# Kernel optimization log

Hardware: AMD Instinct MI355X
Metric: run time of the kernel (lower is better)

## Reference

```python
import jax, jax.numpy as jnp
import numpy as np

B_, N, C = 4096, 49, 128
H = 4          # num_heads
NW = 64        # windows per image


def setup_inputs() -> dict:
    key = jax.random.key(0)
    k = jax.random.split(key, 6)
    s = 0.02
    return {
        "x": jax.random.normal(k[0], (B_, N, C), jnp.float32),
        "mask": jax.random.normal(k[1], (NW, N, N), jnp.float32),
        "qkv_w": jax.random.normal(k[2], (3 * C, C), jnp.float32) * s,
        "qkv_b": jax.random.normal(k[3], (3 * C,), jnp.float32) * s,
        "proj_w": jax.random.normal(k[4], (C, C), jnp.float32) * s,
        "proj_b": jax.random.normal(k[5], (C,), jnp.float32) * s,
    }


def reference(x, mask, qkv_w, qkv_b, proj_w, proj_b):
    b, n, c = x.shape
    hd = c // H
    scale = hd ** -0.5
    # fused QKV projection: [b, n, 3, H, hd] -> [3, b, H, n, hd]
    qkv = (x @ qkv_w.T + qkv_b).reshape(b, n, 3, H, hd)
    qkv = jnp.transpose(qkv, (2, 0, 3, 1, 4))
    q, k, v = qkv[0] * scale, qkv[1], qkv[2]
    attn = jnp.einsum("bhnd,bhmd->bhnm", q, k)  # [b, H, n, n]
    nW = mask.shape[0]
    attn = attn.reshape(b // nW, nW, H, n, n) + mask[None, :, None, :, :]
    attn = jax.nn.softmax(attn.reshape(b, H, n, n), axis=-1)
    out = jnp.einsum("bhnm,bhmd->bhnd", attn, v)
    out = jnp.transpose(out, (0, 2, 1, 3)).reshape(b, n, c)
    return out @ proj_w.T + proj_b
```

## Files before the change

kernel.cpp:

```cpp
#include <hip/hip_runtime.h>
#include <hip/hip_bf16.h>

#define C_DIM 128
#define SCALE 0.17677669529663687f

typedef __attribute__((ext_vector_type(8))) short frag8;
typedef __attribute__((ext_vector_type(4))) float f32x4;
typedef __attribute__((ext_vector_type(4))) unsigned int u32x4;

#define XACT_STR 136
#define VT_BASE 8000
#define VT_PER_HEAD 2304
#define Q_STR 40
#define VT_STR 72
#define SMEM_TOT 17216

__device__ __forceinline__ unsigned short f2b(float x) {
    __hip_bfloat16 h = __float2bfloat16(x);
    return __builtin_bit_cast(unsigned short, h);
}
__device__ __forceinline__ unsigned pk2(float a, float b) {
    return ((unsigned)f2b(b) << 16) | (unsigned)f2b(a);
}
__device__ __forceinline__ void add4(f32x4& a, float4 m) {
    a[0] += m.x; a[1] += m.y; a[2] += m.z; a[3] += m.w;
}

__global__ void convert_weights(const float4* __restrict__ qkvw,
                                const float4* __restrict__ projw,
                                ushort4* __restrict__ wbf) {
    int i = blockIdx.x * 256 + threadIdx.x;
    float4 v = (i < 12288) ? qkvw[i] : projw[i - 12288];
    ushort4 p;
    p.x = f2b(v.x); p.y = f2b(v.y); p.z = f2b(v.z); p.w = f2b(v.w);
    wbf[i] = p;
}

__global__ void pad_mask(const float* __restrict__ mask, float* __restrict__ pm) {
    int t = blockIdx.x * 256 + threadIdx.x;
    int w = t / 784, rem = t % 784, i = rem >> 4, tq = rem & 15;
    const float* src = mask + (size_t)w * 2401 + i * 49;
    int j = tq * 4;
    float4 v;
    v.x = (j     < 49) ? src[j]     : 0.f;
    v.y = (j + 1 < 49) ? src[j + 1] : 0.f;
    v.z = (j + 2 < 49) ? src[j + 2] : 0.f;
    v.w = (j + 3 < 49) ? src[j + 3] : 0.f;
    ((float4*)pm)[t] = v;
}

__global__ __launch_bounds__(256) void attn_mfma(
    const float* __restrict__ x,
    const float* __restrict__ pmask,
    const float* __restrict__ qkv_b,
    const float* __restrict__ proj_b,
    const unsigned short* __restrict__ wq,
    float* __restrict__ out)
{
    __shared__ __align__(16) unsigned short sm[SMEM_TOT];

    const int b = blockIdx.x, tid = threadIdx.x;
    const int h    = tid >> 6;
    const int lane = tid & 63;
    const int n16  = lane & 15;
    const int q    = lane >> 4;

    {
        const float4* xg = (const float4*)(x + (size_t)b * 6272);
        for (int i = tid; i < 1568; i += 256) {
            float4 v = xg[i];
            int row = i >> 5, col = (i & 31) << 2;
            uint2 pk; pk.x = pk2(v.x, v.y); pk.y = pk2(v.z, v.w);
            *(uint2*)&sm[row * XACT_STR + col] = pk;
        }
    }
    __syncthreads();

    frag8 xf[4][4];
#pragma unroll
    for (int tt = 0; tt < 4; ++tt)
#pragma unroll
        for (int ks = 0; ks < 4; ++ks)
            xf[tt][ks] = *(const frag8*)&sm[min(tt * 16 + n16, 48) * XACT_STR + ks * 32 + q * 8];
    __syncthreads();

    const int KB = h * 2000;
    const int VB = VT_BASE + h * VT_PER_HEAD;

#pragma unroll
    for (int ct = 0; ct < 2; ++ct) {
        const unsigned short* wrow = wq + (size_t)(C_DIM + h * 32 + ct * 16 + n16) * C_DIM;
        frag8 wf[4];
#pragma unroll
        for (int ks = 0; ks < 4; ++ks) wf[ks] = *(const frag8*)(wrow + ks * 32 + q * 8);
        float4 b4 = *(const float4*)(qkv_b + C_DIM + h * 32 + ct * 16 + q * 4);
#pragma unroll
        for (int tt = 0; tt < 4; ++tt) {
            f32x4 acc = {0.f, 0.f, 0.f, 0.f};
#pragma unroll
            for (int ks = 0; ks < 4; ++ks)
                acc = __builtin_amdgcn_mfma_f32_16x16x32_bf16(wf[ks], xf[tt][ks], acc, 0, 0, 0);
            uint2 pk;
            pk.x = pk2(acc[0] + b4.x, acc[1] + b4.y);
            pk.y = pk2(acc[2] + b4.z, acc[3] + b4.w);
            *(uint2*)&sm[KB + min(tt * 16 + n16, 49) * Q_STR + ct * 16 + q * 4] = pk;
        }
    }
#pragma unroll
    for (int ct = 0; ct < 2; ++ct) {
        const unsigned short* wrow = wq + (size_t)(2 * C_DIM + h * 32 + ct * 16 + n16) * C_DIM;
        frag8 wf[4];
#pragma unroll
        for (int ks = 0; ks < 4; ++ks) wf[ks] = *(const frag8*)(wrow + ks * 32 + q * 8);
        float bias = qkv_b[2 * C_DIM + h * 32 + ct * 16 + n16];
#pragma unroll
        for (int tt = 0; tt < 4; ++tt) {
            f32x4 acc = {0.f, 0.f, 0.f, 0.f};
#pragma unroll
            for (int ks = 0; ks < 4; ++ks)
                acc = __builtin_amdgcn_mfma_f32_16x16x32_bf16(xf[tt][ks], wf[ks], acc, 0, 0, 0);
            uint2 pk;
            pk.x = pk2(acc[0] + bias, acc[1] + bias);
            pk.y = pk2(acc[2] + bias, acc[3] + bias);
            *(uint2*)&sm[VB + (ct * 16 + n16) * VT_STR + tt * 16 + q * 4] = pk;
        }
    }
    unsigned qw[4][2][2];
#pragma unroll
    for (int ct = 0; ct < 2; ++ct) {
        const unsigned short* wrow = wq + (size_t)(h * 32 + ct * 16 + n16) * C_DIM;
        frag8 wf[4];
#pragma unroll
        for (int ks = 0; ks < 4; ++ks) wf[ks] = *(const frag8*)(wrow + ks * 32 + q * 8);
        float4 b4 = *(const float4*)(qkv_b + h * 32 + ct * 16 + q * 4);
#pragma unroll
        for (int tt = 0; tt < 4; ++tt) {
            f32x4 acc = {0.f, 0.f, 0.f, 0.f};
#pragma unroll
            for (int ks = 0; ks < 4; ++ks)
                acc = __builtin_amdgcn_mfma_f32_16x16x32_bf16(wf[ks], xf[tt][ks], acc, 0, 0, 0);
            qw[tt][ct][0] = pk2((acc[0] + b4.x) * SCALE, (acc[1] + b4.y) * SCALE);
            qw[tt][ct][1] = pk2((acc[2] + b4.z) * SCALE, (acc[3] + b4.w) * SCALE);
        }
    }

    const int srcA = ((q & 1) << 5) + n16;
    const int srcB = srcA + 16;
    const int hi = q >> 1;
    frag8 qf[4];
#pragma unroll
    for (int it = 0; it < 4; ++it) {
        unsigned a00 = __shfl((int)qw[it][0][0], srcA);
        unsigned a10 = __shfl((int)qw[it][1][0], srcA);
        unsigned a01 = __shfl((int)qw[it][0][1], srcA);
        unsigned a11 = __shfl((int)qw[it][1][1], srcA);
        unsigned b00 = __shfl((int)qw[it][0][0], srcB);
        unsigned b10 = __shfl((int)qw[it][1][0], srcB);
        unsigned b01 = __shfl((int)qw[it][0][1], srcB);
        unsigned b11 = __shfl((int)qw[it][1][1], srcB);
        u32x4 t;
        t[0] = hi ? a10 : a00;
        t[1] = hi ? a11 : a01;
        t[2] = hi ? b10 : b00;
        t[3] = hi ? b11 : b01;
        qf[it] = __builtin_bit_cast(frag8, t);
    }

    frag8 kf[4];
#pragma unroll
    for (int t = 0; t < 4; ++t)
        kf[t] = *(const frag8*)&sm[KB + (t * 16 + n16) * Q_STR + q * 8];
    frag8 vf[2][2];
#pragma unroll
    for (int ct = 0; ct < 2; ++ct)
#pragma unroll
        for (int ks = 0; ks < 2; ++ks)
            vf[ct][ks] = *(const frag8*)&sm[VB + (ct * 16 + n16) * VT_STR + ks * 32 + q * 8];
    __syncthreads();

    const float4* pm4 = (const float4*)(pmask + (size_t)(b & 63) * 3136);
    f32x4 o[2][4];
#pragma unroll
    for (int ct = 0; ct < 2; ++ct)
#pragma unroll
        for (int nt = 0; nt < 4; ++nt) o[ct][nt] = (f32x4){0.f, 0.f, 0.f, 0.f};

#pragma unroll
    for (int it = 0; it < 4; ++it) {
        int ii = min(it * 16 + n16, 48);
        float4 mj[4];
#pragma unroll
        for (int jt = 0; jt < 4; ++jt) mj[jt] = pm4[ii * 16 + q + jt * 4];

        f32x4 s4[4];
#pragma unroll
        for (int jt = 0; jt < 4; ++jt) {
            s4[jt] = (f32x4){0.f, 0.f, 0.f, 0.f};
            s4[jt] = __builtin_amdgcn_mfma_f32_16x16x32_bf16(kf[jt], qf[it], s4[jt], 0, 0, 0);
        }
#pragma unroll
        for (int jt = 0; jt < 4; ++jt) add4(s4[jt], mj[jt]);

        float mx = -1e30f;
#pragma unroll
        for (int jt = 0; jt < 4; ++jt)
#pragma unroll
            for (int r = 0; r < 4; ++r)
                if (jt * 16 + q * 4 + r < 49) mx = fmaxf(mx, s4[jt][r]);
        mx = fmaxf(mx, __shfl_xor(mx, 16));
        mx = fmaxf(mx, __shfl_xor(mx, 32));

        float sum = 0.f;
#pragma unroll
        for (int jt = 0; jt < 4; ++jt)
#pragma unroll
            for (int r = 0; r < 4; ++r) {
                float e = (jt * 16 + q * 4 + r < 49) ? __expf(s4[jt][r] - mx) : 0.f;
                s4[jt][r] = e;
                sum += e;
            }
        sum += __shfl_xor(sum, 16);
        sum += __shfl_xor(sum, 32);
        float inv = __builtin_amdgcn_rcpf(sum);

        unsigned pw[4][2];
#pragma unroll
        for (int jt = 0; jt < 4; ++jt) {
            pw[jt][0] = pk2(s4[jt][0], s4[jt][1]);
            pw[jt][1] = pk2(s4[jt][2], s4[jt][3]);
        }
#pragma unroll
        for (int ks = 0; ks < 2; ++ks) {
            unsigned a0  = __shfl((int)pw[2 * ks][0],     srcA);
            unsigned a0h = __shfl((int)pw[2 * ks + 1][0], srcA);
            unsigned a1  = __shfl((int)pw[2 * ks][1],     srcA);
            unsigned a1h = __shfl((int)pw[2 * ks + 1][1], srcA);
            unsigned b0  = __shfl((int)pw[2 * ks][0],     srcB);
            unsigned b0h = __shfl((int)pw[2 * ks + 1][0], srcB);
            unsigned b1  = __shfl((int)pw[2 * ks][1],     srcB);
            unsigned b1h = __shfl((int)pw[2 * ks + 1][1], srcB);
            u32x4 t;
            t[0] = hi ? a0h : a0;
            t[1] = hi ? a1h : a1;
            t[2] = hi ? b0h : b0;
            t[3] = hi ? b1h : b1;
            frag8 pf = __builtin_bit_cast(frag8, t);
#pragma unroll
            for (int ct = 0; ct < 2; ++ct)
                o[ct][it] = __builtin_amdgcn_mfma_f32_16x16x32_bf16(vf[ct][ks], pf, o[ct][it], 0, 0, 0);
        }
#pragma unroll
        for (int ct = 0; ct < 2; ++ct)
#pragma unroll
            for (int r = 0; r < 4; ++r) o[ct][it][r] *= inv;
    }

#pragma unroll
    for (int ct = 0; ct < 2; ++ct)
#pragma unroll
        for (int nt = 0; nt < 4; ++nt) {
            uint2 pk;
            pk.x = pk2(o[ct][nt][0], o[ct][nt][1]);
            pk.y = pk2(o[ct][nt][2], o[ct][nt][3]);
            *(uint2*)&sm[min(nt * 16 + n16, 49) * XACT_STR + h * 32 + ct * 16 + q * 4] = pk;
        }

    const unsigned short* pwq = wq + 49152;
    frag8 wf2[2][4];
#pragma unroll
    for (int ct = 0; ct < 2; ++ct)
#pragma unroll
        for (int ks = 0; ks < 4; ++ks)
            wf2[ct][ks] = *(const frag8*)(pwq + (size_t)(h * 32 + ct * 16 + n16) * C_DIM + ks * 32 + q * 8);
    float4 pb4[2];
#pragma unroll
    for (int ct = 0; ct < 2; ++ct)
        pb4[ct] = *(const float4*)(proj_b + h * 32 + ct * 16 + q * 4);
    __syncthreads();

    float* outb = out + (size_t)b * 6272;
    frag8 af[4][4];
#pragma unroll
    for (int nt = 0; nt < 4; ++nt)
#pragma unroll
        for (int ks = 0; ks < 4; ++ks)
            af[nt][ks] = *(const frag8*)&sm[min(nt * 16 + n16, 48) * XACT_STR + ks * 32 + q * 8];
#pragma unroll
    for (int nt = 0; nt < 4; ++nt) {
        int tok = nt * 16 + n16;
#pragma unroll
        for (int ct = 0; ct < 2; ++ct) {
            f32x4 acc = {0.f, 0.f, 0.f, 0.f};
#pragma unroll
            for (int ks = 0; ks < 4; ++ks)
                acc = __builtin_amdgcn_mfma_f32_16x16x32_bf16(wf2[ct][ks], af[nt][ks], acc, 0, 0, 0);
            if (tok < 49)
                *(float4*)&outb[tok * C_DIM + h * 32 + ct * 16 + q * 4] =
                    make_float4(acc[0] + pb4[ct].x, acc[1] + pb4[ct].y,
                                acc[2] + pb4[ct].z, acc[3] + pb4[ct].w);
        }
    }
}

extern "C" void kernel_launch(void* const* d_in, const int* in_sizes, int n_in,
                              void* d_out, int out_size, void* d_ws, size_t ws_size,
                              hipStream_t stream) {
    const float* x      = (const float*)d_in[0];
    const float* mask   = (const float*)d_in[1];
    const float* qkv_b  = (const float*)d_in[3];
    const float* proj_b = (const float*)d_in[5];

    unsigned short* wbf = (unsigned short*)d_ws;
    float* pmask = (float*)((char*)d_ws + 131072);
    convert_weights<<<64, 256, 0, stream>>>((const float4*)d_in[2],
                                            (const float4*)d_in[4],
                                            (ushort4*)wbf);
    pad_mask<<<196, 256, 0, stream>>>(mask, pmask);
    attn_mfma<<<4096, 256, 0, stream>>>(x, pmask, qkv_b, proj_b, wbf, (float*)d_out);
}
```

Before: 270.0 us.

## Split each head across two wavefronts by token tiles, doubling block size

Each block now runs 512 threads, with two wavefronts per head that each own half of the 16-row token tiles for the QKV projection, attention and output projection. A separate shared-memory region holds the attention output, so it no longer overwrites the x staging area, and a barrier is added after the K/V writes. The aim is more parallelism and latency hiding per window with fewer registers per wave. In exchange, each wave reloads the same weight fragments, more shared memory is used per block, and K/V now have to be exchanged between the two waves.

```diff
diff --git a/kernel.cpp b/kernel.cpp
--- a/kernel.cpp
+++ b/kernel.cpp
@@ -11,9 +11,10 @@
 #define XACT_STR 136
 #define VT_BASE 8000
 #define VT_PER_HEAD 2304
+#define ACT_BASE 17216
 #define Q_STR 40
 #define VT_STR 72
-#define SMEM_TOT 17216
+#define SMEM_TOT 24016
 
 __device__ __forceinline__ unsigned short f2b(float x) {
     __hip_bfloat16 h = __float2bfloat16(x);
@@ -49,7 +50,7 @@
     ((float4*)pm)[t] = v;
 }
 
-__global__ __launch_bounds__(256) void attn_mfma(
+__global__ __launch_bounds__(512) void attn_mfma(
     const float* __restrict__ x,
     const float* __restrict__ pmask,
     const float* __restrict__ qkv_b,
@@ -60,14 +61,17 @@
     __shared__ __align__(16) unsigned short sm[SMEM_TOT];
 
     const int b = blockIdx.x, tid = threadIdx.x;
-    const int h    = tid >> 6;
+    const int w    = tid >> 6;
+    const int h    = w >> 1;
+    const int half = w & 1;
+    const int t0   = half * 2;
     const int lane = tid & 63;
     const int n16  = lane & 15;
     const int q    = lane >> 4;
 
     {
         const float4* xg = (const float4*)(x + (size_t)b * 6272);
-        for (int i = tid; i < 1568; i += 256) {
+        for (int i = tid; i < 1568; i += 512) {
             float4 v = xg[i];
             int row = i >> 5, col = (i & 31) << 2;
             uint2 pk; pk.x = pk2(v.x, v.y); pk.y = pk2(v.z, v.w);
@@ -76,12 +80,12 @@
     }
     __syncthreads();
 
-    frag8 xf[4][4];
-#pragma unroll
-    for (int tt = 0; tt < 4; ++tt)
+    frag8 xf[2][4];
+#pragma unroll
+    for (int il = 0; il < 2; ++il)
 #pragma unroll
         for (int ks = 0; ks < 4; ++ks)
-            xf[tt][ks] = *(const frag8*)&sm[min(tt * 16 + n16, 48) * XACT_STR + ks * 32 + q * 8];
+            xf[il][ks] = *(const frag8*)&sm[min((t0 + il) * 16 + n16, 48) * XACT_STR + ks * 32 + q * 8];
     __syncthreads();
 
     const int KB = h * 2000;
@@ -95,15 +99,15 @@
         for (int ks = 0; ks < 4; ++ks) wf[ks] = *(const frag8*)(wrow + ks * 32 + q * 8);
         float4 b4 = *(const float4*)(qkv_b + C_DIM + h * 32 + ct * 16 + q * 4);
 #pragma unroll
-        for (int tt = 0; tt < 4; ++tt) {
+        for (int il = 0; il < 2; ++il) {
             f32x4 acc = {0.f, 0.f, 0.f, 0.f};
 #pragma unroll
             for (int ks = 0; ks < 4; ++ks)
-                acc = __builtin_amdgcn_mfma_f32_16x16x32_bf16(wf[ks], xf[tt][ks], acc, 0, 0, 0);
+                acc = __builtin_amdgcn_mfma_f32_16x16x32_bf16(wf[ks], xf[il][ks], acc, 0, 0, 0);
             uint2 pk;
             pk.x = pk2(acc[0] + b4.x, acc[1] + b4.y);
             pk.y = pk2(acc[2] + b4.z, acc[3] + b4.w);
-            *(uint2*)&sm[KB + min(tt * 16 + n16, 49) * Q_STR + ct * 16 + q * 4] = pk;
+            *(uint2*)&sm[KB + min((t0 + il) * 16 + n16, 49) * Q_STR + ct * 16 + q * 4] = pk;
         }
     }
 #pragma unroll
@@ -114,18 +118,18 @@
         for (int ks = 0; ks < 4; ++ks) wf[ks] = *(const frag8*)(wrow + ks * 32 + q * 8);
         float bias = qkv_b[2 * C_DIM + h * 32 + ct * 16 + n16];
 #pragma unroll
-        for (int tt = 0; tt < 4; ++tt) {
+        for (int il = 0; il < 2; ++il) {
             f32x4 acc = {0.f, 0.f, 0.f, 0.f};
 #pragma unroll
             for (int ks = 0; ks < 4; ++ks)
-                acc = __builtin_amdgcn_mfma_f32_16x16x32_bf16(xf[tt][ks], wf[ks], acc, 0, 0, 0);
+                acc = __builtin_amdgcn_mfma_f32_16x16x32_bf16(xf[il][ks], wf[ks], acc, 0, 0, 0);
             uint2 pk;
             pk.x = pk2(acc[0] + bias, acc[1] + bias);
             pk.y = pk2(acc[2] + bias, acc[3] + bias);
-            *(uint2*)&sm[VB + (ct * 16 + n16) * VT_STR + tt * 16 + q * 4] = pk;
-        }
-    }
-    unsigned qw[4][2][2];
+            *(uint2*)&sm[VB + (ct * 16 + n16) * VT_STR + (t0 + il) * 16 + q * 4] = pk;
+        }
+    }
+    unsigned qw[2][2][2];
 #pragma unroll
     for (int ct = 0; ct < 2; ++ct) {
         const unsigned short* wrow = wq + (size_t)(h * 32 + ct * 16 + n16) * C_DIM;
@@ -134,36 +138,37 @@
         for (int ks = 0; ks < 4; ++ks) wf[ks] = *(const frag8*)(wrow + ks * 32 + q * 8);
         float4 b4 = *(const float4*)(qkv_b + h * 32 + ct * 16 + q * 4);
 #pragma unroll
-        for (int tt = 0; tt < 4; ++tt) {
+        for (int il = 0; il < 2; ++il) {
             f32x4 acc = {0.f, 0.f, 0.f, 0.f};
 #pragma unroll
             for (int ks = 0; ks < 4; ++ks)
-                acc = __builtin_amdgcn_mfma_f32_16x16x32_bf16(wf[ks], xf[tt][ks], acc, 0, 0, 0);
-            qw[tt][ct][0] = pk2((acc[0] + b4.x) * SCALE, (acc[1] + b4.y) * SCALE);
-            qw[tt][ct][1] = pk2((acc[2] + b4.z) * SCALE, (acc[3] + b4.w) * SCALE);
-        }
-    }
+                acc = __builtin_amdgcn_mfma_f32_16x16x32_bf16(wf[ks], xf[il][ks], acc, 0, 0, 0);
+            qw[il][ct][0] = pk2((acc[0] + b4.x) * SCALE, (acc[1] + b4.y) * SCALE);
+            qw[il][ct][1] = pk2((acc[2] + b4.z) * SCALE, (acc[3] + b4.w) * SCALE);
+        }
+    }
+    __syncthreads();
 
     const int srcA = ((q & 1) << 5) + n16;
     const int srcB = srcA + 16;
     const int hi = q >> 1;
-    frag8 qf[4];
-#pragma unroll
-    for (int it = 0; it < 4; ++it) {
-        unsigned a00 = __shfl((int)qw[it][0][0], srcA);
-        unsigned a10 = __shfl((int)qw[it][1][0], srcA);
-        unsigned a01 = __shfl((int)qw[it][0][1], srcA);
-        unsigned a11 = __shfl((int)qw[it][1][1], srcA);
-        unsigned b00 = __shfl((int)qw[it][0][0], srcB);
-        unsigned b10 = __shfl((int)qw[it][1][0], srcB);
-        unsigned b01 = __shfl((int)qw[it][0][1], srcB);
-        unsigned b11 = __shfl((int)qw[it][1][1], srcB);
+    frag8 qf[2];
+#pragma unroll
+    for (int il = 0; il < 2; ++il) {
+        unsigned a00 = __shfl((int)qw[il][0][0], srcA);
+        unsigned a10 = __shfl((int)qw[il][1][0], srcA);
+        unsigned a01 = __shfl((int)qw[il][0][1], srcA);
+        unsigned a11 = __shfl((int)qw[il][1][1], srcA);
+        unsigned b00 = __shfl((int)qw[il][0][0], srcB);
+        unsigned b10 = __shfl((int)qw[il][1][0], srcB);
+        unsigned b01 = __shfl((int)qw[il][0][1], srcB);
+        unsigned b11 = __shfl((int)qw[il][1][1], srcB);
         u32x4 t;
         t[0] = hi ? a10 : a00;
         t[1] = hi ? a11 : a01;
         t[2] = hi ? b10 : b00;
         t[3] = hi ? b11 : b01;
-        qf[it] = __builtin_bit_cast(frag8, t);
+        qf[il] = __builtin_bit_cast(frag8, t);
     }
 
     frag8 kf[4];
@@ -176,17 +181,17 @@
 #pragma unroll
         for (int ks = 0; ks < 2; ++ks)
             vf[ct][ks] = *(const frag8*)&sm[VB + (ct * 16 + n16) * VT_STR + ks * 32 + q * 8];
-    __syncthreads();
 
     const float4* pm4 = (const float4*)(pmask + (size_t)(b & 63) * 3136);
-    f32x4 o[2][4];
-#pragma unroll
-    for (int ct = 0; ct < 2; ++ct)
-#pragma unroll
-        for (int nt = 0; nt < 4; ++nt) o[ct][nt] = (f32x4){0.f, 0.f, 0.f, 0.f};
-
-#pragma unroll
-    for (int it = 0; it < 4; ++it) {
+    f32x4 o[2][2];
+#pragma unroll
+    for (int ct = 0; ct < 2; ++ct)
+#pragma unroll
+        for (int il = 0; il < 2; ++il) o[ct][il] = (f32x4){0.f, 0.f, 0.f, 0.f};
+
+#pragma unroll
+    for (int il = 0; il < 2; ++il) {
+        const int it = t0 + il;
         int ii = min(it * 16 + n16, 48);
         float4 mj[4];
 #pragma unroll
@@ -196,7 +201,7 @@
 #pragma unroll
         for (int jt = 0; jt < 4; ++jt) {
             s4[jt] = (f32x4){0.f, 0.f, 0.f, 0.f};
-            s4[jt] = __builtin_amdgcn_mfma_f32_16x16x32_bf16(kf[jt], qf[it], s4[jt], 0, 0, 0);
+            s4[jt] = __builtin_amdgcn_mfma_f32_16x16x32_bf16(kf[jt], qf[il], s4[jt], 0, 0, 0);
         }
 #pragma unroll
         for (int jt = 0; jt < 4; ++jt) add4(s4[jt], mj[jt]);
@@ -247,22 +252,22 @@
             frag8 pf = __builtin_bit_cast(frag8, t);
 #pragma unroll
             for (int ct = 0; ct < 2; ++ct)
-                o[ct][it] = __builtin_amdgcn_mfma_f32_16x16x32_bf16(vf[ct][ks], pf, o[ct][it], 0, 0, 0);
+                o[ct][il] = __builtin_amdgcn_mfma_f32_16x16x32_bf16(vf[ct][ks], pf, o[ct][il], 0, 0, 0);
         }
 #pragma unroll
         for (int ct = 0; ct < 2; ++ct)
 #pragma unroll
-            for (int r = 0; r < 4; ++r) o[ct][it][r] *= inv;
-    }
-
-#pragma unroll
-    for (int ct = 0; ct < 2; ++ct)
-#pragma unroll
-        for (int nt = 0; nt < 4; ++nt) {
+            for (int r = 0; r < 4; ++r) o[ct][il][r] *= inv;
+    }
+
+#pragma unroll
+    for (int ct = 0; ct < 2; ++ct)
+#pragma unroll
+        for (int il = 0; il < 2; ++il) {
             uint2 pk;
-            pk.x = pk2(o[ct][nt][0], o[ct][nt][1]);
-            pk.y = pk2(o[ct][nt][2], o[ct][nt][3]);
-            *(uint2*)&sm[min(nt * 16 + n16, 49) * XACT_STR + h * 32 + ct * 16 + q * 4] = pk;
+            pk.x = pk2(o[ct][il][0], o[ct][il][1]);
+            pk.y = pk2(o[ct][il][2], o[ct][il][3]);
+            *(uint2*)&sm[ACT_BASE + min((t0 + il) * 16 + n16, 49) * XACT_STR + h * 32 + ct * 16 + q * 4] = pk;
         }
 
     const unsigned short* pwq = wq + 49152;
@@ -279,21 +284,20 @@
     __syncthreads();
 
     float* outb = out + (size_t)b * 6272;
-    frag8 af[4][4];
-#pragma unroll
-    for (int nt = 0; nt < 4; ++nt)
+#pragma unroll
+    for (int il = 0; il < 2; ++il) {
+        const int nt = t0 + il;
+        frag8 af[4];
 #pragma unroll
         for (int ks = 0; ks < 4; ++ks)
-            af[nt][ks] = *(const frag8*)&sm[min(nt * 16 + n16, 48) * XACT_STR + ks * 32 + q * 8];
-#pragma unroll
-    for (int nt = 0; nt < 4; ++nt) {
+            af[ks] = *(const frag8*)&sm[ACT_BASE + min(nt * 16 + n16, 48) * XACT_STR + ks * 32 + q * 8];
         int tok = nt * 16 + n16;
 #pragma unroll
         for (int ct = 0; ct < 2; ++ct) {
             f32x4 acc = {0.f, 0.f, 0.f, 0.f};
 #pragma unroll
             for (int ks = 0; ks < 4; ++ks)
-                acc = __builtin_amdgcn_mfma_f32_16x16x32_bf16(wf2[ct][ks], af[nt][ks], acc, 0, 0, 0);
+                acc = __builtin_amdgcn_mfma_f32_16x16x32_bf16(wf2[ct][ks], af[ks], acc, 0, 0, 0);
             if (tok < 49)
                 *(float4*)&outb[tok * C_DIM + h * 32 + ct * 16 + q * 4] =
                     make_float4(acc[0] + pb4[ct].x, acc[1] + pb4[ct].y,
@@ -316,5 +320,5 @@
                                             (const float4*)d_in[4],
                                             (ushort4*)wbf);
     pad_mask<<<196, 256, 0, stream>>>(mask, pmask);
-    attn_mfma<<<4096, 256, 0, stream>>>(x, pmask, qkv_b, proj_b, wbf, (float*)d_out);
-}
+    attn_mfma<<<4096, 512, 0, stream>>>(x, pmask, qkv_b, proj_b, wbf, (float*)d_out);
+}
```

Measured after the change: 303.2 us. 1.12x slower.
